# Kernel optimization log

Measured on AMD Instinct MI355X. Metric: run time of the kernel, lower is better.

## Reference

```python
import jax, jax.numpy as jnp
import numpy as np
from jax import lax

ALPHA = 4.0  # spikingjelly default Sigmoid surrogate alpha
EPS = 1e-5

@jax.custom_vjp
def spike_fn(u):
    return (u >= 0.0).astype(u.dtype)

def _spike_fwd(u):
    return spike_fn(u), u

def _spike_bwd(u, g):
    sg = jax.nn.sigmoid(ALPHA * u)
    return (g * ALPHA * sg * (1.0 - sg),)

spike_fn.defvjp(_spike_fwd, _spike_bwd)

def if_node(x):
    """Multi-step IF neuron (v_threshold=1, hard reset to 0) over leading T dim."""
    def step(v, xt):
        v = v + xt
        s = spike_fn(v - 1.0)
        v = v * (1.0 - s)
        return v, s
    _, spikes = lax.scan(step, jnp.zeros_like(x[0]), x)
    return spikes

def layer_norm(x, g, b):
    m = jnp.mean(x, axis=-1, keepdims=True)
    var = jnp.mean((x - m) ** 2, axis=-1, keepdims=True)
    return (x - m) * lax.rsqrt(var + EPS) * g + b

def setup_inputs() -> dict:
    key = jax.random.key(0)
    T, B, S, D = 4, 8, 1024, 768
    ks = jax.random.split(key, 5)
    scale = 1.0 / np.sqrt(D)
    inp = {
        "x": jax.random.normal(ks[0], (T, B, S, D), jnp.float32),
        "wq": jax.random.normal(ks[1], (D, D), jnp.float32) * scale,
        "wk": jax.random.normal(ks[2], (D, D), jnp.float32) * scale,
        "wv": jax.random.normal(ks[3], (D, D), jnp.float32) * scale,
        "wo": jax.random.normal(ks[4], (D, D), jnp.float32) * scale,
        "gq": jnp.ones((D,), jnp.float32), "bq": jnp.zeros((D,), jnp.float32),
        "gk": jnp.ones((D,), jnp.float32), "bk": jnp.zeros((D,), jnp.float32),
        "gv": jnp.ones((D,), jnp.float32), "bv": jnp.zeros((D,), jnp.float32),
        "go": jnp.ones((D,), jnp.float32), "bo": jnp.zeros((D,), jnp.float32),
    }
    return inp

def reference(x, wq, wk, wv, wo, gq, bq, gk, bk, gv, bv, go, bo):
    T, B, S, D = x.shape
    H, HD = 12, 64
    tmp = if_node(x)                                   # [T,B,S,D] spikes
    Q = if_node(layer_norm(tmp @ wq, gq, bq))
    K = if_node(layer_norm(tmp @ wk, gk, bk))
    V = if_node(layer_norm(tmp @ wv, gv, bv))
    # [T,B,S,H,HD] -> [T,B,H,S,HD]
    Q = Q.reshape(T, B, S, H, HD).transpose(0, 1, 3, 2, 4)
    K = K.reshape(T, B, S, H, HD).transpose(0, 1, 3, 2, 4)
    V = V.reshape(T, B, S, H, HD).transpose(0, 1, 3, 2, 4)
    QK = jnp.sum(Q * K, axis=-2, keepdims=True)        # [T,B,H,1,HD]
    QK = if_node(QK)                                   # talking_heads IF spikes
    QKV = V * QK                                       # broadcast over S
    QKV = QKV.transpose(0, 1, 3, 2, 4).reshape(T, B, S, D)
    return layer_norm(QKV @ wo, go, bo)
```

## Files before the change

### kernel.cpp

```cpp
#include <hip/hip_runtime.h>
#include <hip/hip_bf16.h>

#define T_ 4
#define B_ 8
#define S_ 1024
#define D_ 768
#define BS_ (B_*S_)
#define M_ (T_*B_*S_)
#define BSD_ (B_*S_*D_)
#define LN_EPS 1e-5f
#define TAU 4e-5f

typedef unsigned short u16;
typedef unsigned char u8;
typedef unsigned long long u64;
typedef __bf16 bf16x8 __attribute__((ext_vector_type(8)));
typedef float f32x4 __attribute__((ext_vector_type(4)));

__global__ __launch_bounds__(768)
void k_if_mask(const float* __restrict__ x, u64* __restrict__ Am, u16* __restrict__ Ab) {
    int bs = blockIdx.x;
    int d = threadIdx.x;
    int wv = d >> 6, lane = d & 63;
    float v = 0.f;
    for (int t = 0; t < T_; ++t) {
        v += x[(size_t)t * BSD_ + (size_t)bs * D_ + d];
        bool s = (v >= 1.0f);
        u64 m = __ballot(s);
        if (lane == 0) Am[((size_t)t * 12 + wv) * BS_ + bs] = m;
        Ab[(size_t)t * BSD_ + (size_t)bs * D_ + d] = s ? 0x3F80 : 0;
        if (s) v = 0.f;
    }
}

__global__ void k_wconv(const float* __restrict__ wq, const float* __restrict__ wk,
                        const float* __restrict__ wv, const float* __restrict__ wo,
                        u16* __restrict__ Whi, u16* __restrict__ Wlo, u16* __restrict__ Wo) {
    int idx = blockIdx.x * 256 + threadIdx.x;
    int mat = idx / (D_ * D_);
    int r = idx % (D_ * D_);
    int n = r / D_;
    int k = r % D_;
    const float* src = (mat == 0) ? wq : (mat == 1) ? wk : (mat == 2) ? wv : wo;
    float w = src[k * D_ + n];
    __bf16 hi = (__bf16)w;
    u16 uhi = __builtin_bit_cast(u16, hi);
    if (mat == 3) { Wo[r] = uhi; return; }
    float lo = w - (float)hi;
    u16 ulo = __builtin_bit_cast(u16, (__bf16)lo);
    Whi[(size_t)mat * D_ * D_ + r] = uhi;
    Wlo[(size_t)mat * D_ * D_ + r] = ulo;
}

__device__ __forceinline__ void gload16(const void* g, void* l) {
    __builtin_amdgcn_global_load_lds(
        (const __attribute__((address_space(1))) unsigned int*)g,
        (__attribute__((address_space(3))) unsigned int*)l, 16, 0, 0);
}

template<int NMATS>
__global__ __launch_bounds__(256)
void k_gemm(const u16* __restrict__ A, const u16* __restrict__ Bhi,
            const u16* __restrict__ Blo, float* __restrict__ C, int ntn, int N) {
    __shared__ __align__(16) u16 As[128 * 32];
    __shared__ __align__(16) u16 Bh[128 * 32];
    __shared__ __align__(16) u16 Bl[128 * 32];
    int bid = blockIdx.x;
    bid = (bid & 7) * (gridDim.x >> 3) + (bid >> 3);
    int bn = bid % ntn, bm = bid / ntn;
    int tid = threadIdx.x;
    int l = tid & 63, w = tid >> 6;
    int wr = w >> 1, wc = w & 1;
    int lan16 = l & 15, kh = l >> 4;

    f32x4 acc[4][4];
    #pragma unroll
    for (int m = 0; m < 4; ++m)
        #pragma unroll
        for (int n = 0; n < 4; ++n)
            #pragma unroll
            for (int r = 0; r < 4; ++r) acc[m][n][r] = 0.f;

    int arow = bm * 128 + (tid >> 2);
    int brow = bn * 128 + (tid >> 2);
    int colb = (((tid & 3) ^ ((tid >> 3) & 3)) * 8);
    char* ldsA = (char*)As + ((tid >> 6) << 10);
    char* ldsBh = (char*)Bh + ((tid >> 6) << 10);
    char* ldsBl = (char*)Bl + ((tid >> 6) << 10);

    int khs16 = (kh ^ ((lan16 >> 1) & 3)) << 4;
    int aoff[4], boff[4];
    #pragma unroll
    for (int m = 0; m < 4; ++m) aoff[m] = (wr * 64 + m * 16 + lan16) * 64 + khs16;
    #pragma unroll
    for (int n = 0; n < 4; ++n) boff[n] = (wc * 64 + n * 16 + lan16) * 64 + khs16;

    for (int kk = 0; kk < 768; kk += 32) {
        gload16(A   + (size_t)(arow     ) * 768 + kk + colb, ldsA);
        gload16(A   + (size_t)(arow + 64) * 768 + kk + colb, ldsA + 4096);
        gload16(Bhi + (size_t)(brow     ) * 768 + kk + colb, ldsBh);
        gload16(Bhi + (size_t)(brow + 64) * 768 + kk + colb, ldsBh + 4096);
        if (NMATS == 2) {
            gload16(Blo + (size_t)(brow     ) * 768 + kk + colb, ldsBl);
            gload16(Blo + (size_t)(brow + 64) * 768 + kk + colb, ldsBl + 4096);
        }
        __syncthreads();
        bf16x8 af[4], bh[4], bl[4];
        #pragma unroll
        for (int m = 0; m < 4; ++m)
            af[m] = *(const bf16x8*)((const char*)As + aoff[m]);
        #pragma unroll
        for (int n = 0; n < 4; ++n) {
            bh[n] = *(const bf16x8*)((const char*)Bh + boff[n]);
            if (NMATS == 2) bl[n] = *(const bf16x8*)((const char*)Bl + boff[n]);
        }
        #pragma unroll
        for (int m = 0; m < 4; ++m)
            #pragma unroll
            for (int n = 0; n < 4; ++n) {
                acc[m][n] = __builtin_amdgcn_mfma_f32_16x16x32_bf16(af[m], bh[n], acc[m][n], 0, 0, 0);
                if (NMATS == 2)
                    acc[m][n] = __builtin_amdgcn_mfma_f32_16x16x32_bf16(af[m], bl[n], acc[m][n], 0, 0, 0);
            }
        __syncthreads();
    }
    #pragma unroll
    for (int m = 0; m < 4; ++m)
        #pragma unroll
        for (int n = 0; n < 4; ++n)
            #pragma unroll
            for (int r = 0; r < 4; ++r) {
                int crow = bm * 128 + wr * 64 + m * 16 + kh * 4 + r;
                int ccol = bn * 128 + wc * 64 + n * 16 + lan16;
                C[(size_t)crow * N + ccol] = acc[m][n][r];
            }
}

__global__ __launch_bounds__(256)
void k_lnif(const float* __restrict__ Y, const float* __restrict__ g,
            const float* __restrict__ bt, u8* __restrict__ Sp, u8* __restrict__ flag) {
    #pragma clang fp contract(off)
    int row = blockIdx.x * 4 + (threadIdx.x >> 6);
    int lane = threadIdx.x & 63;
    float v[12];
    #pragma unroll
    for (int i = 0; i < 12; ++i) v[i] = 0.f;
    float gv[12], bv[12];
    #pragma unroll
    for (int i = 0; i < 12; ++i) { gv[i] = g[lane + 64*i]; bv[i] = bt[lane + 64*i]; }
    bool fl = false;
    for (int t = 0; t < T_; ++t) {
        size_t base = ((size_t)t * BS_ + row) * D_;
        float xv[12];
        double s = 0.0;
        #pragma unroll
        for (int i = 0; i < 12; ++i) { xv[i] = Y[base + lane + 64*i]; s += (double)xv[i]; }
        #pragma unroll
        for (int o = 1; o < 64; o <<= 1) s += __shfl_xor(s, o, 64);
        s = __shfl(s, 0, 64);
        float m = (float)(s / 768.0);
        float d[12];
        double q = 0.0;
        #pragma unroll
        for (int i = 0; i < 12; ++i) { d[i] = xv[i] - m; float sq = d[i]*d[i]; q += (double)sq; }
        #pragma unroll
        for (int o = 1; o < 64; o <<= 1) q += __shfl_xor(q, o, 64);
        q = __shfl(q, 0, 64);
        float var = (float)(q / 768.0);
        float inv = 1.0f / __fsqrt_rn(var + LN_EPS);
        #pragma unroll
        for (int i = 0; i < 12; ++i) {
            float yn = ((d[i] * inv) * gv[i]) + bv[i];
            v[i] += yn;
            fl = fl || (fabsf(v[i] - 1.0f) < TAU);
            bool sp = (v[i] >= 1.0f);
            Sp[base + lane + 64*i] = sp ? (u8)1 : (u8)0;
            if (sp) v[i] = 0.f;
        }
    }
    u64 bal = __ballot(fl);
    if (lane == 0 && bal != 0ull) flag[row] = 1;
}

__global__ __launch_bounds__(192)
void k_repair(const u64* __restrict__ Am,
              const float* __restrict__ wq, const float* __restrict__ wk,
              const float* __restrict__ wv,
              const float* __restrict__ gq, const float* __restrict__ bq,
              const float* __restrict__ gk, const float* __restrict__ bk,
              const float* __restrict__ gv, const float* __restrict__ bv,
              u8* __restrict__ Qs, u8* __restrict__ Ks, u8* __restrict__ Vs,
              const u8* __restrict__ flags) {
    #pragma clang fp contract(off)
    int mat = blockIdx.y;
    int bs = blockIdx.x;
    if (!flags[(size_t)mat * BS_ + bs]) return;
    const float* W = (mat == 0) ? wq : (mat == 1) ? wk : wv;
    const float* g = (mat == 0) ? gq : (mat == 1) ? gk : gv;
    const float* bb = (mat == 0) ? bq : (mat == 1) ? bk : bv;
    u8* Sp = (mat == 0) ? Qs : (mat == 1) ? Ks : Vs;
    const float4* Wv4 = (const float4*)W;
    __shared__ double red[3];
    __shared__ u64 mword_s[12];
    __shared__ int pops_s[12];
    __shared__ int cnt_s;
    __shared__ u16 idxs[768];
    int c = threadIdx.x;
    int wv_ = c >> 6, lane = c & 63;
    float4 gd = ((const float4*)g)[c];
    float4 bd = ((const float4*)bb)[c];
    float v0 = 0.f, v1 = 0.f, v2 = 0.f, v3 = 0.f;
    for (int t = 0; t < T_; ++t) {
        if (c < 12) {
            u64 m = Am[((size_t)t * 12 + c) * BS_ + bs];
            mword_s[c] = m;
            pops_s[c] = __popcll(m);
        }
        __syncthreads();
        if (c < 12) {
            int off = 0;
            for (int j = 0; j < c; ++j) off += pops_s[j];
            u64 m = mword_s[c];
            int base = c * 64;
            while (m) {
                int kb = __builtin_ctzll(m);
                m &= m - 1;
                idxs[off++] = (u16)(base + kb);
            }
            if (c == 11) cnt_s = off;
        }
        __syncthreads();
        int cnt = cnt_s;
        float y0 = 0.f, y1 = 0.f, y2 = 0.f, y3 = 0.f;
        #pragma unroll 8
        for (int i = 0; i < cnt; ++i) {
            float4 w = Wv4[(size_t)idxs[i] * 192 + c];
            y0 += w.x; y1 += w.y; y2 += w.z; y3 += w.w;
        }
        double s = (double)y0 + (double)y1 + (double)y2 + (double)y3;
        #pragma unroll
        for (int o = 1; o < 64; o <<= 1) s += __shfl_xor(s, o, 64);
        if (lane == 0) red[wv_] = s;
        __syncthreads();
        double stot = red[0] + red[1] + red[2];
        float mean = (float)(stot / 768.0);
        float d0 = y0 - mean, d1 = y1 - mean, d2 = y2 - mean, d3 = y3 - mean;
        double q = (double)(d0*d0) + (double)(d1*d1) + (double)(d2*d2) + (double)(d3*d3);
        #pragma unroll
        for (int o = 1; o < 64; o <<= 1) q += __shfl_xor(q, o, 64);
        __syncthreads();
        if (lane == 0) red[wv_] = q;
        __syncthreads();
        double qtot = red[0] + red[1] + red[2];
        float var = (float)(qtot / 768.0);
        float inv = 1.0f / __fsqrt_rn(var + LN_EPS);
        uchar4 o4;
        {
            float yn = ((d0 * inv) * gd.x) + bd.x; v0 += yn;
            bool sp = (v0 >= 1.0f); o4.x = sp ? 1 : 0; if (sp) v0 = 0.f;
        }
        {
            float yn = ((d1 * inv) * gd.y) + bd.y; v1 += yn;
            bool sp = (v1 >= 1.0f); o4.y = sp ? 1 : 0; if (sp) v1 = 0.f;
        }
        {
            float yn = ((d2 * inv) * gd.z) + bd.z; v2 += yn;
            bool sp = (v2 >= 1.0f); o4.z = sp ? 1 : 0; if (sp) v2 = 0.f;
        }
        {
            float yn = ((d3 * inv) * gd.w) + bd.w; v3 += yn;
            bool sp = (v3 >= 1.0f); o4.w = sp ? 1 : 0; if (sp) v3 = 0.f;
        }
        *(uchar4*)(Sp + ((size_t)t * BS_ + bs) * D_ + c * 4) = o4;
        __syncthreads();
    }
}

__global__ void k_qkred(const u8* __restrict__ Q, const u8* __restrict__ K,
                        float* __restrict__ QK) {
    int bid = blockIdx.x;
    int sg = bid & 31, tb = bid >> 5;
    int tid = threadIdx.x;
    int c4 = tid * 4;
    size_t base = (size_t)tb * S_ * D_ + (size_t)sg * 32 * D_;
    int acc[4] = {0, 0, 0, 0};
    for (int s = 0; s < 32; ++s) {
        uchar4 q = *(const uchar4*)(Q + base + (size_t)s * D_ + c4);
        uchar4 k = *(const uchar4*)(K + base + (size_t)s * D_ + c4);
        acc[0] += q.x & k.x; acc[1] += q.y & k.y; acc[2] += q.z & k.z; acc[3] += q.w & k.w;
    }
    float* dst = QK + (size_t)tb * D_ + c4;
    #pragma unroll
    for (int j = 0; j < 4; ++j) atomicAdd(dst + j, (float)acc[j]);
}

__global__ void k_qkif(const float* __restrict__ QK, u8* __restrict__ QKs) {
    int i = blockIdx.x * 256 + threadIdx.x;
    float v = 0.f;
    for (int t = 0; t < T_; ++t) {
        v += QK[t * (B_ * D_) + i];
        bool s = (v >= 1.0f);
        QKs[t * (B_ * D_) + i] = s ? 1 : 0;
        if (s) v = 0.f;
    }
}

__global__ void k_qkv(const u8* __restrict__ V, const u8* __restrict__ QKs,
                      u16* __restrict__ O) {
    size_t e = ((size_t)blockIdx.x * 256 + threadIdx.x) * 4;
    uchar4 v = *(const uchar4*)(V + e);
    size_t d = e % D_;
    size_t b = (e / ((size_t)S_ * D_)) % B_;
    size_t t = e / BSD_;
    uchar4 qk = *(const uchar4*)(QKs + t * (B_ * D_) + b * D_ + d);
    ushort4 o;
    o.x = (v.x & qk.x) ? 0x3F80 : 0;
    o.y = (v.y & qk.y) ? 0x3F80 : 0;
    o.z = (v.z & qk.z) ? 0x3F80 : 0;
    o.w = (v.w & qk.w) ? 0x3F80 : 0;
    *(ushort4*)(O + e) = o;
}

__device__ __forceinline__ float block_sum(float v, float* red) {
    #pragma unroll
    for (int o = 32; o > 0; o >>= 1) v += __shfl_down(v, o, 64);
    int lane = threadIdx.x & 63, w = threadIdx.x >> 6;
    __syncthreads();
    if (lane == 0) red[w] = v;
    __syncthreads();
    return (red[0] + red[1]) + (red[2] + red[3]);
}

__global__ __launch_bounds__(256)
void k_lnfinal(const float* __restrict__ Y, const float* __restrict__ g,
               const float* __restrict__ bt, float* __restrict__ out) {
    #pragma clang fp contract(off)
    __shared__ float red[4];
    size_t row = (size_t)blockIdx.x * D_;
    int tid = threadIdx.x;
    float y[3];
    float s = 0.f;
    #pragma unroll
    for (int j = 0; j < 3; ++j) { y[j] = Y[row + tid + j * 256]; s += y[j]; }
    float mean = block_sum(s, red) / 768.0f;
    float q = 0.f;
    #pragma unroll
    for (int j = 0; j < 3; ++j) { float d = y[j] - mean; q += d * d; }
    float var = block_sum(q, red) / 768.0f;
    float inv = 1.0f / __fsqrt_rn(var + LN_EPS);
    #pragma unroll
    for (int j = 0; j < 3; ++j) {
        int c = tid + j * 256;
        out[row + c] = (y[j] - mean) * inv * g[c] + bt[c];
    }
}

extern "C" void kernel_launch(void* const* d_in, const int* in_sizes, int n_in,
                              void* d_out, int out_size, void* d_ws, size_t ws_size,
                              hipStream_t stream) {
    const float* x  = (const float*)d_in[0];
    const float* wq = (const float*)d_in[1];
    const float* wk = (const float*)d_in[2];
    const float* wv = (const float*)d_in[3];
    const float* wo = (const float*)d_in[4];
    const float* gq = (const float*)d_in[5];
    const float* bq = (const float*)d_in[6];
    const float* gk = (const float*)d_in[7];
    const float* bk = (const float*)d_in[8];
    const float* gv = (const float*)d_in[9];
    const float* bv = (const float*)d_in[10];
    const float* go = (const float*)d_in[11];
    const float* bo = (const float*)d_in[12];
    float* out = (float*)d_out;

    char* ws = (char*)d_ws;
    size_t off = 0;
    auto alloc = [&](size_t bytes) -> void* {
        void* p = ws + off;
        off += (bytes + 255) & ~(size_t)255;
        return p;
    };
    u64* Am    = (u64*)alloc((size_t)T_ * 12 * BS_ * 8);
    u16* Ab    = (u16*)alloc((size_t)M_ * D_ * 2);
    float* Y   = (float*)alloc((size_t)M_ * D_ * 4);
    u8* Qs     = (u8*)alloc((size_t)M_ * D_);
    u8* Ks     = (u8*)alloc((size_t)M_ * D_);
    u8* Vs     = (u8*)alloc((size_t)M_ * D_);
    u16* Whi   = (u16*)alloc((size_t)3 * D_ * D_ * 2);
    u16* Wlo   = (u16*)alloc((size_t)3 * D_ * D_ * 2);
    u16* Wo    = (u16*)alloc((size_t)D_ * D_ * 2);
    float* QK  = (float*)alloc((size_t)T_ * B_ * D_ * 4);
    u8* QKs    = (u8*)alloc((size_t)T_ * B_ * D_);
    u8* flags  = (u8*)alloc((size_t)3 * BS_);

    hipMemsetAsync(QK, 0, (size_t)T_ * B_ * D_ * 4, stream);
    hipMemsetAsync(flags, 0, (size_t)3 * BS_, stream);

    k_if_mask<<<BS_, 768, 0, stream>>>(x, Am, Ab);
    k_wconv<<<(4 * D_ * D_) / 256, 256, 0, stream>>>(wq, wk, wv, wo, Whi, Wlo, Wo);
    const int ntn = D_ / 128;
    const int gemm_grid = (M_ / 128) * ntn;
    k_gemm<2><<<gemm_grid, 256, 0, stream>>>(Ab, Whi + 0 * D_ * D_, Wlo + 0 * D_ * D_, Y, ntn, D_);
    k_lnif<<<BS_ / 4, 256, 0, stream>>>(Y, gq, bq, Qs, flags + 0 * BS_);
    k_gemm<2><<<gemm_grid, 256, 0, stream>>>(Ab, Whi + 1 * D_ * D_, Wlo + 1 * D_ * D_, Y, ntn, D_);
    k_lnif<<<BS_ / 4, 256, 0, stream>>>(Y, gk, bk, Ks, flags + 1 * BS_);
    k_gemm<2><<<gemm_grid, 256, 0, stream>>>(Ab, Whi + 2 * D_ * D_, Wlo + 2 * D_ * D_, Y, ntn, D_);
    k_lnif<<<BS_ / 4, 256, 0, stream>>>(Y, gv, bv, Vs, flags + 2 * BS_);
    k_repair<<<dim3(BS_, 3), 192, 0, stream>>>(Am, wq, wk, wv, gq, bq, gk, bk, gv, bv,
                                               Qs, Ks, Vs, flags);
    k_qkred<<<T_ * B_ * 32, 192, 0, stream>>>(Qs, Ks, QK);
    k_qkif<<<(B_ * D_) / 256, 256, 0, stream>>>(QK, QKs);
    k_qkv<<<(M_ * D_) / 4 / 256, 256, 0, stream>>>(Vs, QKs, Ab);
    k_gemm<1><<<gemm_grid, 256, 0, stream>>>(Ab, Wo, Wo, Y, ntn, D_);
    k_lnfinal<<<M_, 256, 0, stream>>>(Y, go, bo, out);
}
```

Baseline: 652.7 us.

## Compact flagged rows into a list and repair two rows per block over all timesteps

The LN+IF kernel now appends rows near the spike threshold to a compact per-matrix row list with an atomic counter, replacing a per-row flag array. The repair kernel reads this list, so blocks with no assigned row exit at once instead of all launched blocks checking a flag. Each repair block handles two flagged rows across all four timesteps. It gathers each weight row once over the union of active inputs and routes it to the matching accumulators through a bitmask. This cuts weight reads and block count, at the cost of more registers, divergent adds and more block-wide reductions per block.

```diff
diff --git a/kernel.cpp b/kernel.cpp
--- a/kernel.cpp
+++ b/kernel.cpp
@@ -13,6 +13,7 @@
 
 typedef unsigned short u16;
 typedef unsigned char u8;
+typedef unsigned int u32;
 typedef unsigned long long u64;
 typedef __bf16 bf16x8 __attribute__((ext_vector_type(8)));
 typedef float f32x4 __attribute__((ext_vector_type(4)));
@@ -138,7 +139,8 @@
 
 __global__ __launch_bounds__(256)
 void k_lnif(const float* __restrict__ Y, const float* __restrict__ g,
-            const float* __restrict__ bt, u8* __restrict__ Sp, u8* __restrict__ flag) {
+            const float* __restrict__ bt, u8* __restrict__ Sp,
+            int* __restrict__ rowlist, int* __restrict__ cnt, int mat) {
     #pragma clang fp contract(off)
     int row = blockIdx.x * 4 + (threadIdx.x >> 6);
     int lane = threadIdx.x & 63;
@@ -179,100 +181,170 @@
         }
     }
     u64 bal = __ballot(fl);
-    if (lane == 0 && bal != 0ull) flag[row] = 1;
+    if (lane == 0 && bal != 0ull) {
+        int slot = atomicAdd(cnt + mat, 1);
+        rowlist[mat * BS_ + slot] = row;
+    }
+}
+
+__device__ __forceinline__ double bred192(double v, double* red) {
+    #pragma unroll
+    for (int o = 1; o < 64; o <<= 1) v += __shfl_xor(v, o, 64);
+    int lane = threadIdx.x & 63, w = threadIdx.x >> 6;
+    __syncthreads();
+    if (lane == 0) red[w] = v;
+    __syncthreads();
+    return red[0] + red[1] + red[2];
 }
 
 __global__ __launch_bounds__(192)
-void k_repair(const u64* __restrict__ Am,
-              const float* __restrict__ wq, const float* __restrict__ wk,
-              const float* __restrict__ wv,
-              const float* __restrict__ gq, const float* __restrict__ bq,
-              const float* __restrict__ gk, const float* __restrict__ bk,
-              const float* __restrict__ gv, const float* __restrict__ bv,
-              u8* __restrict__ Qs, u8* __restrict__ Ks, u8* __restrict__ Vs,
-              const u8* __restrict__ flags) {
+void k_repairU(const u64* __restrict__ Am,
+               const float* __restrict__ wq, const float* __restrict__ wk,
+               const float* __restrict__ wv,
+               const float* __restrict__ gq, const float* __restrict__ bq,
+               const float* __restrict__ gk, const float* __restrict__ bk,
+               const float* __restrict__ gv, const float* __restrict__ bv,
+               u8* __restrict__ Qs, u8* __restrict__ Ks, u8* __restrict__ Vs,
+               const int* __restrict__ rowlist, const int* __restrict__ cnt) {
     #pragma clang fp contract(off)
     int mat = blockIdx.y;
-    int bs = blockIdx.x;
-    if (!flags[(size_t)mat * BS_ + bs]) return;
+    int nf = cnt[mat];
+    int base = blockIdx.x * 2;
+    if (base >= nf) return;
     const float* W = (mat == 0) ? wq : (mat == 1) ? wk : wv;
     const float* g = (mat == 0) ? gq : (mat == 1) ? gk : gv;
     const float* bb = (mat == 0) ? bq : (mat == 1) ? bk : bv;
     u8* Sp = (mat == 0) ? Qs : (mat == 1) ? Ks : Vs;
     const float4* Wv4 = (const float4*)W;
+
+    __shared__ u64 mks[2][4][12];
+    __shared__ u64 uni[12];
+    __shared__ int pops[12];
+    __shared__ u16 idxs[768];
+    __shared__ u8 tms[768];
+    __shared__ int cnt_s;
     __shared__ double red[3];
-    __shared__ u64 mword_s[12];
-    __shared__ int pops_s[12];
-    __shared__ int cnt_s;
-    __shared__ u16 idxs[768];
-    int c = threadIdx.x;
-    int wv_ = c >> 6, lane = c & 63;
+    __shared__ int rows_s[2];
+
+    int tid = threadIdx.x;
+    if (tid < 2) {
+        int e = base + tid;
+        rows_s[tid] = rowlist[mat * BS_ + (e < nf ? e : nf - 1)];
+    }
+    __syncthreads();
+    int r0 = rows_s[0], r1 = rows_s[1];
+    if (tid < 96) {
+        int rr = tid / 48, rem = tid % 48;
+        int t = rem / 12, kw = rem % 12;
+        int row = rr ? r1 : r0;
+        mks[rr][t][kw] = Am[((size_t)t * 12 + kw) * BS_ + row];
+    }
+    __syncthreads();
+    if (tid < 12) {
+        u64 u = 0;
+        #pragma unroll
+        for (int rr = 0; rr < 2; ++rr)
+            #pragma unroll
+            for (int t = 0; t < 4; ++t) u |= mks[rr][t][tid];
+        uni[tid] = u;
+        pops[tid] = __popcll(u);
+    }
+    __syncthreads();
+    if (tid < 12) {
+        int off = 0;
+        for (int j = 0; j < tid; ++j) off += pops[j];
+        u64 u = uni[tid];
+        int kb0 = tid * 64;
+        while (u) {
+            int kb = __builtin_ctzll(u);
+            u &= u - 1;
+            u8 tm = 0;
+            #pragma unroll
+            for (int rr = 0; rr < 2; ++rr)
+                #pragma unroll
+                for (int t = 0; t < 4; ++t)
+                    tm |= (u8)(((mks[rr][t][tid] >> kb) & 1ull) << (rr * 4 + t));
+            idxs[off] = (u16)(kb0 + kb);
+            tms[off] = tm;
+            ++off;
+        }
+        if (tid == 11) cnt_s = off;
+    }
+    __syncthreads();
+    int cu = cnt_s;
+
+    int c = tid;
     float4 gd = ((const float4*)g)[c];
     float4 bd = ((const float4*)bb)[c];
-    float v0 = 0.f, v1 = 0.f, v2 = 0.f, v3 = 0.f;
-    for (int t = 0; t < T_; ++t) {
-        if (c < 12) {
-            u64 m = Am[((size_t)t * 12 + c) * BS_ + bs];
-            mword_s[c] = m;
-            pops_s[c] = __popcll(m);
-        }
-        __syncthreads();
-        if (c < 12) {
-            int off = 0;
-            for (int j = 0; j < c; ++j) off += pops_s[j];
-            u64 m = mword_s[c];
-            int base = c * 64;
-            while (m) {
-                int kb = __builtin_ctzll(m);
-                m &= m - 1;
-                idxs[off++] = (u16)(base + kb);
+
+    float y[2][4][4];
+    #pragma unroll
+    for (int rr = 0; rr < 2; ++rr)
+        #pragma unroll
+        for (int t = 0; t < 4; ++t)
+            #pragma unroll
+            for (int j = 0; j < 4; ++j) y[rr][t][j] = 0.f;
+
+    #pragma unroll 2
+    for (int i = 0; i < cu; ++i) {
+        int k = idxs[i];
+        int tm = tms[i];
+        float4 w = Wv4[(size_t)k * 192 + c];
+        if (tm & 1)   { y[0][0][0] += w.x; y[0][0][1] += w.y; y[0][0][2] += w.z; y[0][0][3] += w.w; }
+        if (tm & 2)   { y[0][1][0] += w.x; y[0][1][1] += w.y; y[0][1][2] += w.z; y[0][1][3] += w.w; }
+        if (tm & 4)   { y[0][2][0] += w.x; y[0][2][1] += w.y; y[0][2][2] += w.z; y[0][2][3] += w.w; }
+        if (tm & 8)   { y[0][3][0] += w.x; y[0][3][1] += w.y; y[0][3][2] += w.z; y[0][3][3] += w.w; }
+        if (tm & 16)  { y[1][0][0] += w.x; y[1][0][1] += w.y; y[1][0][2] += w.z; y[1][0][3] += w.w; }
+        if (tm & 32)  { y[1][1][0] += w.x; y[1][1][1] += w.y; y[1][1][2] += w.z; y[1][1][3] += w.w; }
+        if (tm & 64)  { y[1][2][0] += w.x; y[1][2][1] += w.y; y[1][2][2] += w.z; y[1][2][3] += w.w; }
+        if (tm & 128) { y[1][3][0] += w.x; y[1][3][1] += w.y; y[1][3][2] += w.z; y[1][3][3] += w.w; }
+    }
+
+    float mean_[2][4], inv_[2][4];
+    #pragma unroll
+    for (int rr = 0; rr < 2; ++rr)
+        #pragma unroll
+        for (int t = 0; t < 4; ++t) {
+            double s = (double)y[rr][t][0] + (double)y[rr][t][1]
+                     + (double)y[rr][t][2] + (double)y[rr][t][3];
+            double stot = bred192(s, red);
+            float mean = (float)(stot / 768.0);
+            float d0 = y[rr][t][0] - mean, d1 = y[rr][t][1] - mean;
+            float d2 = y[rr][t][2] - mean, d3 = y[rr][t][3] - mean;
+            double q = (double)(d0*d0) + (double)(d1*d1)
+                     + (double)(d2*d2) + (double)(d3*d3);
+            double qtot = bred192(q, red);
+            float var = (float)(qtot / 768.0);
+            mean_[rr][t] = mean;
+            inv_[rr][t] = 1.0f / __fsqrt_rn(var + LN_EPS);
+        }
+
+    #pragma unroll
+    for (int rr = 0; rr < 2; ++rr) {
+        int row = rr ? r1 : r0;
+        uchar4 o4[4];
+        #pragma unroll
+        for (int j = 0; j < 4; ++j) {
+            float gj = (j == 0) ? gd.x : (j == 1) ? gd.y : (j == 2) ? gd.z : gd.w;
+            float bj = (j == 0) ? bd.x : (j == 1) ? bd.y : (j == 2) ? bd.z : bd.w;
+            float v = 0.f;
+            #pragma unroll
+            for (int t = 0; t < 4; ++t) {
+                float d = y[rr][t][j] - mean_[rr][t];
+                float yn = ((d * inv_[rr][t]) * gj) + bj;
+                v += yn;
+                bool sp = (v >= 1.0f);
+                u8 sb = sp ? (u8)1 : (u8)0;
+                if (j == 0) o4[t].x = sb;
+                if (j == 1) o4[t].y = sb;
+                if (j == 2) o4[t].z = sb;
+                if (j == 3) o4[t].w = sb;
+                if (sp) v = 0.f;
             }
-            if (c == 11) cnt_s = off;
-        }
-        __syncthreads();
-        int cnt = cnt_s;
-        float y0 = 0.f, y1 = 0.f, y2 = 0.f, y3 = 0.f;
-        #pragma unroll 8
-        for (int i = 0; i < cnt; ++i) {
-            float4 w = Wv4[(size_t)idxs[i] * 192 + c];
-            y0 += w.x; y1 += w.y; y2 += w.z; y3 += w.w;
-        }
-        double s = (double)y0 + (double)y1 + (double)y2 + (double)y3;
-        #pragma unroll
-        for (int o = 1; o < 64; o <<= 1) s += __shfl_xor(s, o, 64);
-        if (lane == 0) red[wv_] = s;
-        __syncthreads();
-        double stot = red[0] + red[1] + red[2];
-        float mean = (float)(stot / 768.0);
-        float d0 = y0 - mean, d1 = y1 - mean, d2 = y2 - mean, d3 = y3 - mean;
-        double q = (double)(d0*d0) + (double)(d1*d1) + (double)(d2*d2) + (double)(d3*d3);
-        #pragma unroll
-        for (int o = 1; o < 64; o <<= 1) q += __shfl_xor(q, o, 64);
-        __syncthreads();
-        if (lane == 0) red[wv_] = q;
-        __syncthreads();
-        double qtot = red[0] + red[1] + red[2];
-        float var = (float)(qtot / 768.0);
-        float inv = 1.0f / __fsqrt_rn(var + LN_EPS);
-        uchar4 o4;
-        {
-            float yn = ((d0 * inv) * gd.x) + bd.x; v0 += yn;
-            bool sp = (v0 >= 1.0f); o4.x = sp ? 1 : 0; if (sp) v0 = 0.f;
-        }
-        {
-            float yn = ((d1 * inv) * gd.y) + bd.y; v1 += yn;
-            bool sp = (v1 >= 1.0f); o4.y = sp ? 1 : 0; if (sp) v1 = 0.f;
-        }
-        {
-            float yn = ((d2 * inv) * gd.z) + bd.z; v2 += yn;
-            bool sp = (v2 >= 1.0f); o4.z = sp ? 1 : 0; if (sp) v2 = 0.f;
-        }
-        {
-            float yn = ((d3 * inv) * gd.w) + bd.w; v3 += yn;
-            bool sp = (v3 >= 1.0f); o4.w = sp ? 1 : 0; if (sp) v3 = 0.f;
-        }
-        *(uchar4*)(Sp + ((size_t)t * BS_ + bs) * D_ + c * 4) = o4;
-        __syncthreads();
+        }
+        #pragma unroll
+        for (int t = 0; t < 4; ++t)
+            *(uchar4*)(Sp + ((size_t)t * BS_ + row) * D_ + c * 4) = o4[t];
     }
 }
 
@@ -391,23 +463,24 @@
     u16* Wo    = (u16*)alloc((size_t)D_ * D_ * 2);
     float* QK  = (float*)alloc((size_t)T_ * B_ * D_ * 4);
     u8* QKs    = (u8*)alloc((size_t)T_ * B_ * D_);
-    u8* flags  = (u8*)alloc((size_t)3 * BS_);
+    int* rowlist = (int*)alloc((size_t)3 * BS_ * 4);
+    int* cnt   = (int*)alloc(256);
 
     hipMemsetAsync(QK, 0, (size_t)T_ * B_ * D_ * 4, stream);
-    hipMemsetAsync(flags, 0, (size_t)3 * BS_, stream);
+    hipMemsetAsync(cnt, 0, 12, stream);
 
     k_if_mask<<<BS_, 768, 0, stream>>>(x, Am, Ab);
     k_wconv<<<(4 * D_ * D_) / 256, 256, 0, stream>>>(wq, wk, wv, wo, Whi, Wlo, Wo);
     const int ntn = D_ / 128;
     const int gemm_grid = (M_ / 128) * ntn;
     k_gemm<2><<<gemm_grid, 256, 0, stream>>>(Ab, Whi + 0 * D_ * D_, Wlo + 0 * D_ * D_, Y, ntn, D_);
-    k_lnif<<<BS_ / 4, 256, 0, stream>>>(Y, gq, bq, Qs, flags + 0 * BS_);
+    k_lnif<<<BS_ / 4, 256, 0, stream>>>(Y, gq, bq, Qs, rowlist, cnt, 0);
     k_gemm<2><<<gemm_grid, 256, 0, stream>>>(Ab, Whi + 1 * D_ * D_, Wlo + 1 * D_ * D_, Y, ntn, D_);
-    k_lnif<<<BS_ / 4, 256, 0, stream>>>(Y, gk, bk, Ks, flags + 1 * BS_);
+    k_lnif<<<BS_ / 4, 256, 0, stream>>>(Y, gk, bk, Ks, rowlist, cnt, 1);
     k_gemm<2><<<gemm_grid, 256, 0, stream>>>(Ab, Whi + 2 * D_ * D_, Wlo + 2 * D_ * D_, Y, ntn, D_);
-    k_lnif<<<BS_ / 4, 256, 0, stream>>>(Y, gv, bv, Vs, flags + 2 * BS_);
-    k_repair<<<dim3(BS_, 3), 192, 0, stream>>>(Am, wq, wk, wv, gq, bq, gk, bk, gv, bv,
-                                               Qs, Ks, Vs, flags);
+    k_lnif<<<BS_ / 4, 256, 0, stream>>>(Y, gv, bv, Vs, rowlist, cnt, 2);
+    k_repairU<<<dim3(BS_ / 2, 3), 192, 0, stream>>>(Am, wq, wk, wv, gq, bq, gk, bk, gv, bv,
+                                                    Qs, Ks, Vs, rowlist, cnt);
     k_qkred<<<T_ * B_ * 32, 192, 0, stream>>>(Qs, Ks, QK);
     k_qkif<<<(B_ * D_) / 256, 256, 0, stream>>>(QK, QKs);
     k_qkv<<<(M_ * D_) / 4 / 256, 256, 0, stream>>>(Vs, QKs, Ab);
```

Result: slower. 693.2 us (+6.2%).

## Compact flagged rows via atomic list and parallelize repair over timesteps

Applied to the files above, without the earlier changes.

The LN+IF kernel now appends rows that need exact fp32 repair to a compacted row list through an atomic counter, replacing the per-row byte flags. The repair kernel reads that list, so blocks with no work exit after one counter check instead of loading a flag each. Each repair block now computes all four timesteps' sparse row sums in parallel with 768 threads, then one 192-thread group runs the sequential IF recurrence from shared memory. The cost is atomic contention and a larger block that holds more shared memory.

```diff
diff --git a/kernel.cpp b/kernel.cpp
--- a/kernel.cpp
+++ b/kernel.cpp
@@ -13,6 +13,7 @@
 
 typedef unsigned short u16;
 typedef unsigned char u8;
+typedef unsigned int u32;
 typedef unsigned long long u64;
 typedef __bf16 bf16x8 __attribute__((ext_vector_type(8)));
 typedef float f32x4 __attribute__((ext_vector_type(4)));
@@ -138,7 +139,8 @@
 
 __global__ __launch_bounds__(256)
 void k_lnif(const float* __restrict__ Y, const float* __restrict__ g,
-            const float* __restrict__ bt, u8* __restrict__ Sp, u8* __restrict__ flag) {
+            const float* __restrict__ bt, u8* __restrict__ Sp,
+            int* __restrict__ rowlist, int* __restrict__ cnt, int mat) {
     #pragma clang fp contract(off)
     int row = blockIdx.x * 4 + (threadIdx.x >> 6);
     int lane = threadIdx.x & 63;
@@ -179,100 +181,129 @@
         }
     }
     u64 bal = __ballot(fl);
-    if (lane == 0 && bal != 0ull) flag[row] = 1;
-}
-
-__global__ __launch_bounds__(192)
-void k_repair(const u64* __restrict__ Am,
-              const float* __restrict__ wq, const float* __restrict__ wk,
-              const float* __restrict__ wv,
-              const float* __restrict__ gq, const float* __restrict__ bq,
-              const float* __restrict__ gk, const float* __restrict__ bk,
-              const float* __restrict__ gv, const float* __restrict__ bv,
-              u8* __restrict__ Qs, u8* __restrict__ Ks, u8* __restrict__ Vs,
-              const u8* __restrict__ flags) {
+    if (lane == 0 && bal != 0ull) {
+        int slot = atomicAdd(cnt + mat, 1);
+        rowlist[mat * BS_ + slot] = row;
+    }
+}
+
+__global__ __launch_bounds__(768)
+void k_repairT(const u64* __restrict__ Am,
+               const float* __restrict__ wq, const float* __restrict__ wk,
+               const float* __restrict__ wv,
+               const float* __restrict__ gq, const float* __restrict__ bq,
+               const float* __restrict__ gk, const float* __restrict__ bk,
+               const float* __restrict__ gv, const float* __restrict__ bv,
+               u8* __restrict__ Qs, u8* __restrict__ Ks, u8* __restrict__ Vs,
+               const int* __restrict__ rowlist, const int* __restrict__ cnt) {
     #pragma clang fp contract(off)
     int mat = blockIdx.y;
-    int bs = blockIdx.x;
-    if (!flags[(size_t)mat * BS_ + bs]) return;
+    if (blockIdx.x >= cnt[mat]) return;
+    int row = rowlist[mat * BS_ + blockIdx.x];
     const float* W = (mat == 0) ? wq : (mat == 1) ? wk : wv;
     const float* g = (mat == 0) ? gq : (mat == 1) ? gk : gv;
     const float* bb = (mat == 0) ? bq : (mat == 1) ? bk : bv;
     u8* Sp = (mat == 0) ? Qs : (mat == 1) ? Ks : Vs;
     const float4* Wv4 = (const float4*)W;
-    __shared__ double red[3];
-    __shared__ u64 mword_s[12];
-    __shared__ int pops_s[12];
-    __shared__ int cnt_s;
-    __shared__ u16 idxs[768];
-    int c = threadIdx.x;
-    int wv_ = c >> 6, lane = c & 63;
-    float4 gd = ((const float4*)g)[c];
-    float4 bd = ((const float4*)bb)[c];
-    float v0 = 0.f, v1 = 0.f, v2 = 0.f, v3 = 0.f;
-    for (int t = 0; t < T_; ++t) {
-        if (c < 12) {
-            u64 m = Am[((size_t)t * 12 + c) * BS_ + bs];
-            mword_s[c] = m;
-            pops_s[c] = __popcll(m);
+
+    __shared__ u64 mks[4][12];
+    __shared__ int pops[4][12];
+    __shared__ int cnt4[4];
+    __shared__ u16 idxs[4][768];
+    __shared__ float4 ys[4][192];
+    __shared__ float2 mi_sh[4];
+    __shared__ double redd[12];
+
+    int tid = threadIdx.x;
+    int t = tid / 192;
+    int tg = tid % 192;
+
+    if (tid < 48) {
+        int tt = tid / 12, kw = tid % 12;
+        u64 m = Am[((size_t)tt * 12 + kw) * BS_ + row];
+        mks[tt][kw] = m;
+        pops[tt][kw] = __popcll(m);
+    }
+    __syncthreads();
+    if (tid < 48) {
+        int tt = tid / 12, kw = tid % 12;
+        int off = 0;
+        for (int j = 0; j < kw; ++j) off += pops[tt][j];
+        u64 m = mks[tt][kw];
+        int kb0 = kw * 64;
+        while (m) {
+            int kb = __builtin_ctzll(m);
+            m &= m - 1;
+            idxs[tt][off++] = (u16)(kb0 + kb);
         }
-        __syncthreads();
-        if (c < 12) {
-            int off = 0;
-            for (int j = 0; j < c; ++j) off += pops_s[j];
-            u64 m = mword_s[c];
-            int base = c * 64;
-            while (m) {
-                int kb = __builtin_ctzll(m);
-                m &= m - 1;
-                idxs[off++] = (u16)(base + kb);
+        if (kw == 11) cnt4[tt] = off;
+    }
+    __syncthreads();
+
+    int cn = cnt4[t];
+    float y0 = 0.f, y1 = 0.f, y2 = 0.f, y3 = 0.f;
+    const u16* il = idxs[t];
+    #pragma unroll 8
+    for (int i = 0; i < cn; ++i) {
+        float4 w = Wv4[(size_t)il[i] * 192 + tg];
+        y0 += w.x; y1 += w.y; y2 += w.z; y3 += w.w;
+    }
+
+    int lane = tid & 63;
+    int wv_t = tg >> 6;
+    double s = (double)y0 + (double)y1 + (double)y2 + (double)y3;
+    #pragma unroll
+    for (int o = 1; o < 64; o <<= 1) s += __shfl_xor(s, o, 64);
+    if (lane == 0) redd[t * 3 + wv_t] = s;
+    __syncthreads();
+    double stot = redd[t * 3] + redd[t * 3 + 1] + redd[t * 3 + 2];
+    float mean = (float)(stot / 768.0);
+    float d0 = y0 - mean, d1 = y1 - mean, d2 = y2 - mean, d3 = y3 - mean;
+    double q = (double)(d0*d0) + (double)(d1*d1) + (double)(d2*d2) + (double)(d3*d3);
+    #pragma unroll
+    for (int o = 1; o < 64; o <<= 1) q += __shfl_xor(q, o, 64);
+    __syncthreads();
+    if (lane == 0) redd[t * 3 + wv_t] = q;
+    __syncthreads();
+    double qtot = redd[t * 3] + redd[t * 3 + 1] + redd[t * 3 + 2];
+    float var = (float)(qtot / 768.0);
+    float inv = 1.0f / __fsqrt_rn(var + LN_EPS);
+
+    ys[t][tg] = make_float4(y0, y1, y2, y3);
+    if (tg == 0) mi_sh[t] = make_float2(mean, inv);
+    __syncthreads();
+
+    if (tid < 192) {
+        float4 gd = ((const float4*)g)[tg];
+        float4 bd = ((const float4*)bb)[tg];
+        float4 yt[4];
+        float2 mi[4];
+        #pragma unroll
+        for (int tt = 0; tt < 4; ++tt) { yt[tt] = ys[tt][tg]; mi[tt] = mi_sh[tt]; }
+        uchar4 o4[4];
+        #pragma unroll
+        for (int j = 0; j < 4; ++j) {
+            float gj = (j == 0) ? gd.x : (j == 1) ? gd.y : (j == 2) ? gd.z : gd.w;
+            float bj = (j == 0) ? bd.x : (j == 1) ? bd.y : (j == 2) ? bd.z : bd.w;
+            float v = 0.f;
+            #pragma unroll
+            for (int tt = 0; tt < 4; ++tt) {
+                float yj = (j == 0) ? yt[tt].x : (j == 1) ? yt[tt].y : (j == 2) ? yt[tt].z : yt[tt].w;
+                float d = yj - mi[tt].x;
+                float yn = ((d * mi[tt].y) * gj) + bj;
+                v += yn;
+                bool sp = (v >= 1.0f);
+                u8 sb = sp ? (u8)1 : (u8)0;
+                if (j == 0) o4[tt].x = sb;
+                if (j == 1) o4[tt].y = sb;
+                if (j == 2) o4[tt].z = sb;
+                if (j == 3) o4[tt].w = sb;
+                if (sp) v = 0.f;
             }
-            if (c == 11) cnt_s = off;
         }
-        __syncthreads();
-        int cnt = cnt_s;
-        float y0 = 0.f, y1 = 0.f, y2 = 0.f, y3 = 0.f;
-        #pragma unroll 8
-        for (int i = 0; i < cnt; ++i) {
-            float4 w = Wv4[(size_t)idxs[i] * 192 + c];
-            y0 += w.x; y1 += w.y; y2 += w.z; y3 += w.w;
-        }
-        double s = (double)y0 + (double)y1 + (double)y2 + (double)y3;
-        #pragma unroll
-        for (int o = 1; o < 64; o <<= 1) s += __shfl_xor(s, o, 64);
-        if (lane == 0) red[wv_] = s;
-        __syncthreads();
-        double stot = red[0] + red[1] + red[2];
-        float mean = (float)(stot / 768.0);
-        float d0 = y0 - mean, d1 = y1 - mean, d2 = y2 - mean, d3 = y3 - mean;
-        double q = (double)(d0*d0) + (double)(d1*d1) + (double)(d2*d2) + (double)(d3*d3);
-        #pragma unroll
-        for (int o = 1; o < 64; o <<= 1) q += __shfl_xor(q, o, 64);
-        __syncthreads();
-        if (lane == 0) red[wv_] = q;
-        __syncthreads();
-        double qtot = red[0] + red[1] + red[2];
-        float var = (float)(qtot / 768.0);
-        float inv = 1.0f / __fsqrt_rn(var + LN_EPS);
-        uchar4 o4;
-        {
-            float yn = ((d0 * inv) * gd.x) + bd.x; v0 += yn;
-            bool sp = (v0 >= 1.0f); o4.x = sp ? 1 : 0; if (sp) v0 = 0.f;
-        }
-        {
-            float yn = ((d1 * inv) * gd.y) + bd.y; v1 += yn;
-            bool sp = (v1 >= 1.0f); o4.y = sp ? 1 : 0; if (sp) v1 = 0.f;
-        }
-        {
-            float yn = ((d2 * inv) * gd.z) + bd.z; v2 += yn;
-            bool sp = (v2 >= 1.0f); o4.z = sp ? 1 : 0; if (sp) v2 = 0.f;
-        }
-        {
-            float yn = ((d3 * inv) * gd.w) + bd.w; v3 += yn;
-            bool sp = (v3 >= 1.0f); o4.w = sp ? 1 : 0; if (sp) v3 = 0.f;
-        }
-        *(uchar4*)(Sp + ((size_t)t * BS_ + bs) * D_ + c * 4) = o4;
-        __syncthreads();
+        #pragma unroll
+        for (int tt = 0; tt < 4; ++tt)
+            *(uchar4*)(Sp + ((size_t)tt * BS_ + row) * D_ + tg * 4) = o4[tt];
     }
 }
 
@@ -391,23 +422,24 @@
     u16* Wo    = (u16*)alloc((size_t)D_ * D_ * 2);
     float* QK  = (float*)alloc((size_t)T_ * B_ * D_ * 4);
     u8* QKs    = (u8*)alloc((size_t)T_ * B_ * D_);
-    u8* flags  = (u8*)alloc((size_t)3 * BS_);
+    int* rowlist = (int*)alloc((size_t)3 * BS_ * 4);
+    int* cnt   = (int*)alloc(256);
 
     hipMemsetAsync(QK, 0, (size_t)T_ * B_ * D_ * 4, stream);
-    hipMemsetAsync(flags, 0, (size_t)3 * BS_, stream);
+    hipMemsetAsync(cnt, 0, 12, stream);
 
     k_if_mask<<<BS_, 768, 0, stream>>>(x, Am, Ab);
     k_wconv<<<(4 * D_ * D_) / 256, 256, 0, stream>>>(wq, wk, wv, wo, Whi, Wlo, Wo);
     const int ntn = D_ / 128;
     const int gemm_grid = (M_ / 128) * ntn;
     k_gemm<2><<<gemm_grid, 256, 0, stream>>>(Ab, Whi + 0 * D_ * D_, Wlo + 0 * D_ * D_, Y, ntn, D_);
-    k_lnif<<<BS_ / 4, 256, 0, stream>>>(Y, gq, bq, Qs, flags + 0 * BS_);
+    k_lnif<<<BS_ / 4, 256, 0, stream>>>(Y, gq, bq, Qs, rowlist, cnt, 0);
     k_gemm<2><<<gemm_grid, 256, 0, stream>>>(Ab, Whi + 1 * D_ * D_, Wlo + 1 * D_ * D_, Y, ntn, D_);
-    k_lnif<<<BS_ / 4, 256, 0, stream>>>(Y, gk, bk, Ks, flags + 1 * BS_);
+    k_lnif<<<BS_ / 4, 256, 0, stream>>>(Y, gk, bk, Ks, rowlist, cnt, 1);
     k_gemm<2><<<gemm_grid, 256, 0, stream>>>(Ab, Whi + 2 * D_ * D_, Wlo + 2 * D_ * D_, Y, ntn, D_);
-    k_lnif<<<BS_ / 4, 256, 0, stream>>>(Y, gv, bv, Vs, flags + 2 * BS_);
-    k_repair<<<dim3(BS_, 3), 192, 0, stream>>>(Am, wq, wk, wv, gq, bq, gk, bk, gv, bv,
-                                               Qs, Ks, Vs, flags);
+    k_lnif<<<BS_ / 4, 256, 0, stream>>>(Y, gv, bv, Vs, rowlist, cnt, 2);
+    k_repairT<<<dim3(BS_, 3), 768, 0, stream>>>(Am, wq, wk, wv, gq, bq, gk, bk, gv, bv,
+                                                Qs, Ks, Vs, rowlist, cnt);
     k_qkred<<<T_ * B_ * 32, 192, 0, stream>>>(Qs, Ks, QK);
     k_qkif<<<(B_ * D_) / 256, 256, 0, stream>>>(QK, QKs);
     k_qkv<<<(M_ * D_) / 4 / 256, 256, 0, stream>>>(Vs, QKs, Ab);
```

Measured after the change: 593.8 us. 1.1x faster.
